# Kernel optimization log

Measured on AMD Instinct MI355X. Metric: run time of the kernel, lower is better.

## Reference

```python
import jax, jax.numpy as jnp
import numpy as np

B, C, T, D = 4, 248, 500, 64


def setup_inputs() -> dict:
    key = jax.random.key(0)
    ks = jax.random.split(key, 7)
    scale = 1.0  # nn.Linear(1, d) default init is U(-1, 1); exact dist irrelevant for correctness baseline
    return {
        "x": jax.random.normal(ks[0], (B, C, T), dtype=jnp.float32),
        "wq": jax.random.uniform(ks[1], (D,), jnp.float32, -scale, scale),
        "bq": jax.random.uniform(ks[2], (D,), jnp.float32, -scale, scale),
        "wk": jax.random.uniform(ks[3], (D,), jnp.float32, -scale, scale),
        "bk": jax.random.uniform(ks[4], (D,), jnp.float32, -scale, scale),
        "wv": jax.random.uniform(ks[5], (D,), jnp.float32, -scale, scale),
        "bv": jax.random.uniform(ks[6], (D,), jnp.float32, -scale, scale),
    }


def reference(x, wq, bq, wk, bk, wv, bv):
    # x: [B, C, T] -> xt: [B, T, C]; each scalar projected to attn_dim D
    xt = jnp.transpose(x, (0, 2, 1))
    Q = xt[..., None] * wq + bq            # [B, T, C, D]
    K = xt[..., None] * wk + bk            # [B, T, C, D]
    V = xt[..., None] * wv + bv            # [B, T, C, D]
    d = Q.shape[-1]
    # channel-wise attention per (B, T) slice
    scores = jnp.einsum("btcd,bted->btce", Q, K) / jnp.sqrt(jnp.float32(d))
    wts = jax.nn.softmax(scores, axis=-1)  # [B, T, C, C] (dropout=0 / eval mode)
    out = jnp.einsum("btce,bted->btcd", wts, V).mean(axis=2)  # [B, T, D]
    return out, wts
```

## Files before the change

kernel.cpp:

```cpp
#include <hip/hip_runtime.h>
#include <math.h>

#define BB 4
#define CC 248
#define TT 500
#define DD 64
#define NQ (CC * CC / 4)

typedef float f32x4 __attribute__((ext_vector_type(4)));

__global__ __launch_bounds__(256) void csa_kernel(
    const float* __restrict__ x,
    const float* __restrict__ wq, const float* __restrict__ bq,
    const float* __restrict__ wk, const float* __restrict__ bk,
    const float* __restrict__ wv, const float* __restrict__ bv,
    float* __restrict__ out, float* __restrict__ wts)
{
    const int bt = blockIdx.x;
    const int b  = bt / TT;
    const int t  = bt % TT;
    const int tid  = threadIdx.x;
    const int wave = tid >> 6;
    const int lane = tid & 63;

    __shared__ __align__(16) float xs[CC];
    __shared__ __align__(16) f32x4 sRowV[CC];
    __shared__ float sred[8];
    __shared__ float sA, sB2, sXmax, sXmin, sYbar;

    if (tid < CC) xs[tid] = x[((size_t)b * CC + tid) * TT + t];

    if (wave == 1) {
        float wkv = wk[lane];
        float pa = wq[lane] * wkv;
        float pb = bq[lane] * wkv;
        #pragma unroll
        for (int off = 32; off > 0; off >>= 1) {
            pa += __shfl_xor(pa, off, 64);
            pb += __shfl_xor(pb, off, 64);
        }
        if (lane == 0) { sA = pa * 0.125f; sB2 = pb * 0.125f; }
    }
    __syncthreads();

    float vmax = -INFINITY, vmin = INFINITY;
    if (tid < CC) { vmax = xs[tid]; vmin = vmax; }
    #pragma unroll
    for (int off = 32; off > 0; off >>= 1) {
        vmax = fmaxf(vmax, __shfl_xor(vmax, off, 64));
        vmin = fminf(vmin, __shfl_xor(vmin, off, 64));
    }
    if (lane == 0) { sred[wave] = vmax; sred[4 + wave] = vmin; }
    __syncthreads();
    if (tid == 0) {
        sXmax = fmaxf(fmaxf(sred[0], sred[1]), fmaxf(sred[2], sred[3]));
        sXmin = fminf(fminf(sred[4], sred[5]), fminf(sred[6], sred[7]));
    }
    __syncthreads();

    const float LOG2E = 1.4426950408889634f;
    const float a2   = sA  * LOG2E;
    const float b22  = sB2 * LOG2E;
    const float xmax = sXmax;
    const float xmin = sXmin;
    const f32x4* xs4 = reinterpret_cast<const f32x4*>(xs);

    const int  r      = tid;
    const bool rowact = (r < CC);
    const float xr = rowact ? xs[r] : 0.f;
    const float s2 = fmaf(a2, xr, b22);
    const float m2 = (s2 >= 0.f) ? s2 * xmax : s2 * xmin;

    float d0 = 0.f, d1 = 0.f, d2 = 0.f, d3 = 0.f;
    float p0 = 0.f, p1 = 0.f, p2 = 0.f, p3 = 0.f;
    #pragma unroll 2
    for (int j = 0; j < CC / 4; ++j) {
        const f32x4 xv = xs4[j];
        const float e0 = __builtin_amdgcn_exp2f(fmaf(s2, xv.x, -m2));
        const float e1 = __builtin_amdgcn_exp2f(fmaf(s2, xv.y, -m2));
        const float e2 = __builtin_amdgcn_exp2f(fmaf(s2, xv.z, -m2));
        const float e3 = __builtin_amdgcn_exp2f(fmaf(s2, xv.w, -m2));
        d0 += e0; d1 += e1; d2 += e2; d3 += e3;
        p0 = fmaf(e0, xv.x, p0); p1 = fmaf(e1, xv.y, p1);
        p2 = fmaf(e2, xv.z, p2); p3 = fmaf(e3, xv.w, p3);
    }
    const float denom = (d0 + d1) + (d2 + d3);
    const float xp    = (p0 + p1) + (p2 + p3);
    const float inv   = __builtin_amdgcn_rcpf(denom);
    if (rowact) {
        f32x4 prm; prm.x = s2; prm.y = -m2; prm.z = inv; prm.w = 0.f;
        sRowV[r] = prm;
    }

    float yr = rowact ? xp * inv : 0.f;
    #pragma unroll
    for (int off = 32; off > 0; off >>= 1) yr += __shfl_xor(yr, off, 64);
    if (lane == 0) sred[wave] = yr;
    __syncthreads();
    if (tid == 0)
        sYbar = (sred[0] + sred[1] + sred[2] + sred[3]) * (1.0f / CC);
    __syncthreads();

    f32x4* wq4 = reinterpret_cast<f32x4*>(wts + (size_t)bt * (CC * CC));

    #pragma unroll 2
    for (int it = 0; it < NQ / 256; ++it) {
        const int idx = it * 256 + tid;
        const int row = idx / 62;
        const int c4  = idx - row * 62;
        const f32x4 prm = sRowV[row];
        const f32x4 xv  = xs4[c4];
        f32x4 o;
        o.x = __builtin_amdgcn_exp2f(fmaf(prm.x, xv.x, prm.y)) * prm.z;
        o.y = __builtin_amdgcn_exp2f(fmaf(prm.x, xv.y, prm.y)) * prm.z;
        o.z = __builtin_amdgcn_exp2f(fmaf(prm.x, xv.z, prm.y)) * prm.z;
        o.w = __builtin_amdgcn_exp2f(fmaf(prm.x, xv.w, prm.y)) * prm.z;
        wq4[idx] = o;
    }
    {
        const int idx = (NQ / 256) * 256 + tid;
        if (tid < NQ - (NQ / 256) * 256) {
            const int row = idx / 62;
            const int c4  = idx - row * 62;
            const f32x4 prm = sRowV[row];
            const f32x4 xv  = xs4[c4];
            f32x4 o;
            o.x = __builtin_amdgcn_exp2f(fmaf(prm.x, xv.x, prm.y)) * prm.z;
            o.y = __builtin_amdgcn_exp2f(fmaf(prm.x, xv.y, prm.y)) * prm.z;
            o.z = __builtin_amdgcn_exp2f(fmaf(prm.x, xv.z, prm.y)) * prm.z;
            o.w = __builtin_amdgcn_exp2f(fmaf(prm.x, xv.w, prm.y)) * prm.z;
            wq4[idx] = o;
        }
    }

    if (tid < DD)
        out[(size_t)bt * DD + tid] = fmaf(wv[tid], sYbar, bv[tid]);
}

extern "C" void kernel_launch(void* const* d_in, const int* in_sizes, int n_in,
                              void* d_out, int out_size, void* d_ws, size_t ws_size,
                              hipStream_t stream) {
    const float* x  = (const float*)d_in[0];
    const float* wq = (const float*)d_in[1];
    const float* bq = (const float*)d_in[2];
    const float* wk = (const float*)d_in[3];
    const float* bk = (const float*)d_in[4];
    const float* wv = (const float*)d_in[5];
    const float* bv = (const float*)d_in[6];

    float* out = (float*)d_out;
    float* wts = (float*)d_out + (size_t)BB * TT * DD;

    csa_kernel<<<dim3(BB * TT), dim3(256), 0, stream>>>(x, wq, bq, wk, bk, wv, bv, out, wts);
}
```

Baseline: 105.0 us.

## Split into per-row parameter kernel and grid-stride softmax store kernel

Computes per-row softmax parameters (scale, shift, reciprocal denominator) and transposed x in a first kernel, writing them to workspace. A second grid-stride kernel with a fixed 2048-block grid then regenerates and streams out the full weights tensor. The aim is to decouple the bandwidth-bound store from the per-slice reduction work and balance stores across the GPU. The cost is an extra launch plus a workspace round trip, with a fallback to the monolithic kernel when workspace is too small.

```diff
diff --git a/kernel.cpp b/kernel.cpp
--- a/kernel.cpp
+++ b/kernel.cpp
@@ -5,11 +5,130 @@
 #define CC 248
 #define TT 500
 #define DD 64
-#define NQ (CC * CC / 4)
+#define NBT (BB * TT)
+#define QPT (CC * CC / 4)
+#define XTPAD 256
 
 typedef float f32x4 __attribute__((ext_vector_type(4)));
 
-__global__ __launch_bounds__(256) void csa_kernel(
+__global__ __launch_bounds__(256) void csa_params(
+    const float* __restrict__ x,
+    const float* __restrict__ wq, const float* __restrict__ bq,
+    const float* __restrict__ wk, const float* __restrict__ bk,
+    const float* __restrict__ wv, const float* __restrict__ bv,
+    float* __restrict__ out, f32x4* __restrict__ prmOut, float* __restrict__ xtOut)
+{
+    const int bt = blockIdx.x;
+    const int b  = bt / TT;
+    const int t  = bt % TT;
+    const int tid  = threadIdx.x;
+    const int wave = tid >> 6;
+    const int lane = tid & 63;
+
+    __shared__ __align__(16) float xs[CC];
+    __shared__ float sred[8];
+    __shared__ float sA, sB2, sXmax, sXmin;
+
+    if (tid < CC) xs[tid] = x[((size_t)b * CC + tid) * TT + t];
+
+    if (wave == 1) {
+        float wkv = wk[lane];
+        float pa = wq[lane] * wkv;
+        float pb = bq[lane] * wkv;
+        #pragma unroll
+        for (int off = 32; off > 0; off >>= 1) {
+            pa += __shfl_xor(pa, off, 64);
+            pb += __shfl_xor(pb, off, 64);
+        }
+        if (lane == 0) { sA = pa * 0.125f; sB2 = pb * 0.125f; }
+    }
+    __syncthreads();
+
+    float vmax = -INFINITY, vmin = INFINITY;
+    if (tid < CC) { vmax = xs[tid]; vmin = vmax; }
+    #pragma unroll
+    for (int off = 32; off > 0; off >>= 1) {
+        vmax = fmaxf(vmax, __shfl_xor(vmax, off, 64));
+        vmin = fminf(vmin, __shfl_xor(vmin, off, 64));
+    }
+    if (lane == 0) { sred[wave] = vmax; sred[4 + wave] = vmin; }
+    __syncthreads();
+    if (tid == 0) {
+        sXmax = fmaxf(fmaxf(sred[0], sred[1]), fmaxf(sred[2], sred[3]));
+        sXmin = fminf(fminf(sred[4], sred[5]), fminf(sred[6], sred[7]));
+    }
+    __syncthreads();
+
+    const float LOG2E = 1.4426950408889634f;
+    const float a2   = sA  * LOG2E;
+    const float b22  = sB2 * LOG2E;
+    const float xmax = sXmax;
+    const float xmin = sXmin;
+    const f32x4* xs4 = reinterpret_cast<const f32x4*>(xs);
+
+    const int  r      = tid;
+    const bool rowact = (r < CC);
+    const float xr = rowact ? xs[r] : 0.f;
+    const float s2 = fmaf(a2, xr, b22);
+    const float m2 = (s2 >= 0.f) ? s2 * xmax : s2 * xmin;
+
+    float d0 = 0.f, d1 = 0.f, d2 = 0.f, d3 = 0.f;
+    float p0 = 0.f, p1 = 0.f, p2 = 0.f, p3 = 0.f;
+    #pragma unroll 2
+    for (int j = 0; j < CC / 4; ++j) {
+        const f32x4 xv = xs4[j];
+        const float e0 = __builtin_amdgcn_exp2f(fmaf(s2, xv.x, -m2));
+        const float e1 = __builtin_amdgcn_exp2f(fmaf(s2, xv.y, -m2));
+        const float e2 = __builtin_amdgcn_exp2f(fmaf(s2, xv.z, -m2));
+        const float e3 = __builtin_amdgcn_exp2f(fmaf(s2, xv.w, -m2));
+        d0 += e0; d1 += e1; d2 += e2; d3 += e3;
+        p0 = fmaf(e0, xv.x, p0); p1 = fmaf(e1, xv.y, p1);
+        p2 = fmaf(e2, xv.z, p2); p3 = fmaf(e3, xv.w, p3);
+    }
+    const float denom = (d0 + d1) + (d2 + d3);
+    const float xp    = (p0 + p1) + (p2 + p3);
+    const float inv   = __builtin_amdgcn_rcpf(denom);
+
+    if (rowact) {
+        f32x4 prm; prm.x = s2; prm.y = -m2; prm.z = inv; prm.w = 0.f;
+        prmOut[bt * CC + r] = prm;
+    }
+    xtOut[bt * XTPAD + tid] = xr;
+
+    float yr = rowact ? xp * inv : 0.f;
+    #pragma unroll
+    for (int off = 32; off > 0; off >>= 1) yr += __shfl_xor(yr, off, 64);
+    if (lane == 0) sred[wave] = yr;
+    __syncthreads();
+    if (tid < DD) {
+        const float ybar = (sred[0] + sred[1] + sred[2] + sred[3]) * (1.0f / CC);
+        out[(size_t)bt * DD + tid] = fmaf(wv[tid], ybar, bv[tid]);
+    }
+}
+
+__global__ __launch_bounds__(256) void csa_store(
+    const f32x4* __restrict__ prm, const float* __restrict__ xt,
+    f32x4* __restrict__ wq4)
+{
+    const unsigned NQTOT  = (unsigned)NBT * QPT;
+    const unsigned stride = gridDim.x * 256u;
+    for (unsigned idx = blockIdx.x * 256u + threadIdx.x; idx < NQTOT; idx += stride) {
+        const unsigned bt  = idx / QPT;
+        const unsigned rem = idx - bt * QPT;
+        const unsigned row = rem / 62u;
+        const unsigned c4  = rem - row * 62u;
+        const f32x4 p  = prm[bt * CC + row];
+        const f32x4 xv = *reinterpret_cast<const f32x4*>(xt + bt * XTPAD + c4 * 4u);
+        f32x4 o;
+        o.x = __builtin_amdgcn_exp2f(fmaf(p.x, xv.x, p.y)) * p.z;
+        o.y = __builtin_amdgcn_exp2f(fmaf(p.x, xv.y, p.y)) * p.z;
+        o.z = __builtin_amdgcn_exp2f(fmaf(p.x, xv.z, p.y)) * p.z;
+        o.w = __builtin_amdgcn_exp2f(fmaf(p.x, xv.w, p.y)) * p.z;
+        wq4[idx] = o;
+    }
+}
+
+__global__ __launch_bounds__(256) void csa_mono(
     const float* __restrict__ x,
     const float* __restrict__ wq, const float* __restrict__ bq,
     const float* __restrict__ wk, const float* __restrict__ bk,
@@ -101,9 +220,12 @@
         sYbar = (sred[0] + sred[1] + sred[2] + sred[3]) * (1.0f / CC);
     __syncthreads();
 
+    if (tid < DD)
+        out[(size_t)bt * DD + tid] = fmaf(wv[tid], sYbar, bv[tid]);
+
     f32x4* wq4 = reinterpret_cast<f32x4*>(wts + (size_t)bt * (CC * CC));
-
-    #pragma unroll 2
+    const int NQ = QPT;
+    #pragma unroll 4
     for (int it = 0; it < NQ / 256; ++it) {
         const int idx = it * 256 + tid;
         const int row = idx / 62;
@@ -132,9 +254,6 @@
             wq4[idx] = o;
         }
     }
-
-    if (tid < DD)
-        out[(size_t)bt * DD + tid] = fmaf(wv[tid], sYbar, bv[tid]);
 }
 
 extern "C" void kernel_launch(void* const* d_in, const int* in_sizes, int n_in,
@@ -151,5 +270,18 @@
     float* out = (float*)d_out;
     float* wts = (float*)d_out + (size_t)BB * TT * DD;
 
-    csa_kernel<<<dim3(BB * TT), dim3(256), 0, stream>>>(x, wq, bq, wk, bk, wv, bv, out, wts);
-}
+    const size_t prmBytes = (size_t)NBT * CC * sizeof(f32x4);
+    const size_t xtBytes  = (size_t)NBT * XTPAD * sizeof(float);
+
+    if (ws_size >= prmBytes + xtBytes) {
+        f32x4* prm = (f32x4*)d_ws;
+        float* xt  = (float*)((char*)d_ws + prmBytes);
+        csa_params<<<dim3(NBT), dim3(256), 0, stream>>>(
+            x, wq, bq, wk, bk, wv, bv, out, prm, xt);
+        csa_store<<<dim3(2048), dim3(256), 0, stream>>>(
+            prm, xt, reinterpret_cast<f32x4*>(wts));
+    } else {
+        csa_mono<<<dim3(NBT), dim3(256), 0, stream>>>(
+            x, wq, bq, wk, bk, wv, bv, out, wts);
+    }
+}
```

After: 128.9 us. 22.7% more time.
